# Performance work log

Hardware: AMD Instinct MI355X
Metric: run time of the kernel (lower is better)

## Reference

```python
import jax, jax.numpy as jnp
import numpy as np

WS = 32          # window_size -> N = WS*WS = 1024
DIM = 1024
HEADS = 16
BATCH = 16


def _local_mask():
    # token i maps to grid cell (i//WS, i%WS); attend iff within 3x3 neighborhood
    idx = jnp.arange(WS * WS)
    r, c = idx // WS, idx % WS
    return (jnp.abs(r[:, None] - r[None, :]) <= 1) & (jnp.abs(c[:, None] - c[None, :]) <= 1)


def setup_inputs() -> dict:
    key = jax.random.key(0)
    k1, k2, k3 = jax.random.split(key, 3)
    N = WS * WS
    x = jax.random.normal(k1, (BATCH, N, DIM), dtype=jnp.float32)
    w_qkv = jax.random.normal(k2, (3 * DIM, DIM), dtype=jnp.float32) * 0.02
    w_proj = jax.random.normal(k3, (DIM, DIM), dtype=jnp.float32) * 0.02
    b_proj = jnp.zeros((DIM,), dtype=jnp.float32)
    return {"x": x, "w_qkv": w_qkv, "w_proj": w_proj, "b_proj": b_proj}


def reference(x, w_qkv, w_proj, b_proj):
    B, N, C = x.shape
    H = HEADS
    D = C // H
    scale = D ** (-0.5)
    # qkv projection: torch Linear is x @ W^T
    qkv = (x @ w_qkv.T).reshape(B, N, 3, H, D).transpose(2, 0, 3, 1, 4)  # (3,B,H,N,D)
    q, k, v = qkv[0], qkv[1], qkv[2]
    attn = jnp.einsum('bhnd,bhmd->bhnm', q, k) * scale  # (B,H,N,N)
    mask = _local_mask()  # (N,N) bool
    attn = jnp.where(mask[None, None], attn, -jnp.inf)
    attn = jax.nn.softmax(attn, axis=-1)
    out = jnp.einsum('bhnm,bhmd->bhnd', attn, v)          # (B,H,N,D)
    out = out.transpose(0, 2, 1, 3).reshape(B, N, C)      # (B,N,C)
    return out @ w_proj.T + b_proj
```

## Files before the change

kernel.cpp:

```cpp
#include <hip/hip_runtime.h>
#include <hip/hip_bf16.h>
#include <stdint.h>


typedef __bf16 bf16;
typedef __bf16 bf16x4_t __attribute__((ext_vector_type(4)));
typedef __bf16 bf16x8_t __attribute__((ext_vector_type(8)));
typedef float f32x4_t __attribute__((ext_vector_type(4)));

static __device__ __forceinline__ void gload_lds16(const void* g, void* l) {
  __builtin_amdgcn_global_load_lds((__attribute__((address_space(1))) void*)g,
                                   (__attribute__((address_space(3))) void*)l,
                                   16, 0, 0);
}

static __device__ __forceinline__ void block_barrier() {
  asm volatile("" ::: "memory");
  __builtin_amdgcn_s_barrier();
  asm volatile("" ::: "memory");
}

__global__ void cvt_all(const float* __restrict__ x, const float* __restrict__ wq,
                        const float* __restrict__ wp, bf16* __restrict__ xb,
                        bf16* __restrict__ wqb, bf16* __restrict__ wpb) {
  constexpr int NX = 4194304, NWQ = 786432;
  int i = blockIdx.x * blockDim.x + threadIdx.x;
  const float* src; bf16* dst; int off;
  if (i < NX)            { src = x;  dst = xb;  off = i; }
  else if (i < NX + NWQ) { src = wq; dst = wqb; off = i - NX; }
  else                   { src = wp; dst = wpb; off = i - (NX + NWQ); }
  float4 v = reinterpret_cast<const float4*>(src)[off];
  bf16x4_t o;
  o[0] = (bf16)v.x; o[1] = (bf16)v.y; o[2] = (bf16)v.z; o[3] = (bf16)v.w;
  reinterpret_cast<bf16x4_t*>(dst)[off] = o;
}

template<int OUT_BF16>
__global__ __launch_bounds__(256, 2)
void gemm4w(const bf16* __restrict__ A, const bf16* __restrict__ Bm,
            void* __restrict__ Cout, const float* __restrict__ bias,
            int M, int N, int K) {
  constexpr int SLOT = 24576;
  extern __shared__ __align__(16) char lds[];

  const int tid = threadIdx.x;
  const int w = tid >> 6, lane = tid & 63;
  const int fr = lane & 15, g = lane >> 4;
  const int wr = w >> 1, wc = w & 1;

  const int nwg = gridDim.x * gridDim.y;
  int lid = blockIdx.y * gridDim.x + blockIdx.x;
  lid = (lid & 7) * (nwg >> 3) + (lid >> 3);
  const int bx = lid % gridDim.x, by = lid / gridDim.x;
  const int row0 = by * 256, col0 = bx * 128;

  const bf16* Ag = A + (size_t)row0 * K;
  const bf16* Bg = Bm + (size_t)col0 * K;
  const int srow = tid >> 2;
  const int scol = ((tid & 3) ^ ((tid >> 3) & 3)) * 8;
  const int nkt  = K >> 5;

  f32x4_t acc[8][4] = {};

  auto stage = [&](int kt, int slot) {
    const int kb = kt << 5;
    char* sb = lds + slot * SLOT;
#pragma unroll
    for (int n = 0; n < 4; ++n)
      gload_lds16(Ag + (size_t)(n * 64 + srow) * K + kb + scol,
                  sb + n * 4096 + tid * 16);
#pragma unroll
    for (int n = 0; n < 2; ++n)
      gload_lds16(Bg + (size_t)(n * 64 + srow) * K + kb + scol,
                  sb + 16384 + n * 4096 + tid * 16);
  };

  const int uxor = ((fr >> 1) & 3) << 4;

  stage(0, 0);
  stage(1, 1);
  asm volatile("s_waitcnt vmcnt(6)" ::: "memory");
  block_barrier();

  int sl = 0;
  for (int kt = 0; kt < nkt; ++kt) {
    const bool pf = (kt + 2 < nkt);
    int s2 = sl + 2; if (s2 >= 3) s2 -= 3;
    if (pf) stage(kt + 2, s2);
    const char* cA = lds + sl * SLOT;
    const char* cB = cA + 16384;

    bf16x8_t a0[4], a1[4], b0[2], b1[2];
    auto lda = [&](bf16x8_t (&dst)[4], int q) {
#pragma unroll
      for (int i = 0; i < 4; ++i) {
        const int row = wr * 128 + (q * 4 + i) * 16 + fr;
        dst[i] = *reinterpret_cast<const bf16x8_t*>(cA + (row << 6) + ((g << 4) ^ uxor));
      }
    };
    auto ldb = [&](bf16x8_t (&dst)[2], int q) {
#pragma unroll
      for (int j = 0; j < 2; ++j) {
        const int row = wc * 64 + (q * 2 + j) * 16 + fr;
        dst[j] = *reinterpret_cast<const bf16x8_t*>(cB + (row << 6) + ((g << 4) ^ uxor));
      }
    };

    lda(a0, 0);
    ldb(b0, 0);
#pragma unroll
    for (int i = 0; i < 4; ++i)
#pragma unroll
      for (int j = 0; j < 2; ++j)
        acc[i][j] = __builtin_amdgcn_mfma_f32_16x16x32_bf16(a0[i], b0[j], acc[i][j], 0, 0, 0);
    ldb(b1, 1);
#pragma unroll
    for (int i = 0; i < 4; ++i)
#pragma unroll
      for (int j = 0; j < 2; ++j)
        acc[i][2 + j] = __builtin_amdgcn_mfma_f32_16x16x32_bf16(a0[i], b1[j], acc[i][2 + j], 0, 0, 0);
    lda(a1, 1);
#pragma unroll
    for (int i = 0; i < 4; ++i)
#pragma unroll
      for (int j = 0; j < 2; ++j)
        acc[4 + i][2 + j] = __builtin_amdgcn_mfma_f32_16x16x32_bf16(
            a1[i], b1[j], acc[4 + i][2 + j], 0, 0, 0);
#pragma unroll
    for (int i = 0; i < 4; ++i)
#pragma unroll
      for (int j = 0; j < 2; ++j)
        acc[4 + i][j] = __builtin_amdgcn_mfma_f32_16x16x32_bf16(
            a1[i], b0[j], acc[4 + i][j], 0, 0, 0);

    if (pf) asm volatile("s_waitcnt vmcnt(6)" ::: "memory");
    else    asm volatile("s_waitcnt vmcnt(0)" ::: "memory");
    block_barrier();
    sl = (sl + 1 == 3) ? 0 : sl + 1;
  }

#pragma unroll
  for (int fm = 0; fm < 8; ++fm) {
    const int rbase = row0 + wr * 128 + fm * 16 + g * 4;
#pragma unroll
    for (int fn = 0; fn < 4; ++fn) {
      const int col = col0 + wc * 64 + fn * 16 + fr;
#pragma unroll
      for (int r = 0; r < 4; ++r) {
        const size_t idx = (size_t)(rbase + r) * N + col;
        if constexpr (OUT_BF16) {
          reinterpret_cast<bf16*>(Cout)[idx] = (bf16)acc[fm][fn][r];
        } else {
          reinterpret_cast<float*>(Cout)[idx] = acc[fm][fn][r] + bias[col];
        }
      }
    }
  }
}

__global__ __launch_bounds__(256)
void local_attn(const bf16* __restrict__ qkv, bf16* __restrict__ outp) {
  __shared__ __align__(16) char sK[12288];
  __shared__ __align__(16) char sV[12288];

  const int tid  = threadIdx.x;
  const int w = tid >> 6, lane = tid & 63;
  const int ch = lane & 7;
  const int bid = blockIdx.x;
  const int r = bid & 31, h = (bid >> 5) & 15, b = bid >> 9;

  const bf16* qkvb = qkv + (size_t)(b * 1024) * 3072 + h * 64;
  const int tokp = w * 8 + (lane >> 3);

#pragma unroll
  for (int u = 0; u < 3; ++u) {
    const int jrow = min(max(r - 1 + u, 0), 31);
    const size_t j = (size_t)(jrow * 32 + tokp);
    gload_lds16(qkvb + j * 3072 + 1024 + ch * 8, sK + u * 4096 + w * 1024 + (lane & 7) * 16 + (lane >> 3) * 128);
  }
#pragma unroll
  for (int u = 0; u < 3; ++u) {
    const int jrow = min(max(r - 1 + u, 0), 31);
    const size_t j = (size_t)(jrow * 32 + tokp);
    gload_lds16(qkvb + j * 3072 + 2048 + ch * 8, sV + u * 4096 + w * 1024 + (lane & 7) * 16 + (lane >> 3) * 128);
  }

  const int c = tokp, i = r * 32 + c;
  bf16x8_t qv = *reinterpret_cast<const bf16x8_t*>(qkvb + (size_t)i * 3072 + ch * 8);
  float qf[8];
#pragma unroll
  for (int e = 0; e < 8; ++e) qf[e] = (float)qv[e];

  __syncthreads();

  float s[9];
#pragma unroll
  for (int t = 0; t < 9; ++t) {
    const int dr = t / 3 - 1, dc = t % 3 - 1;
    const int rr = r + dr, cc = c + dc;
    const int ccl = min(max(cc, 0), 31);
    const int wtok = (dr + 1) * 32 + ccl;
    const bf16x8_t kvv = *reinterpret_cast<const bf16x8_t*>(sK + wtok * 128 + ch * 16);
    float ps = 0.f;
#pragma unroll
    for (int e = 0; e < 8; ++e) ps += qf[e] * (float)kvv[e];
    ps += __shfl_xor(ps, 1);
    ps += __shfl_xor(ps, 2);
    ps += __shfl_xor(ps, 4);
    const bool valid = (rr >= 0 && rr < 32 && cc >= 0 && cc < 32);
    s[t] = ps * 0.125f + (valid ? 0.f : -1e30f);
  }

  float mx = s[0];
#pragma unroll
  for (int t = 1; t < 9; ++t) mx = fmaxf(mx, s[t]);

  float denom = 0.f, o[8] = {};
#pragma unroll
  for (int t = 0; t < 9; ++t) {
    const int dr = t / 3 - 1, dc = t % 3 - 1;
    const int ccl = min(max(c + dc, 0), 31);
    const int wtok = (dr + 1) * 32 + ccl;
    const float p = __expf(s[t] - mx);
    denom += p;
    const bf16x8_t vvv = *reinterpret_cast<const bf16x8_t*>(sV + wtok * 128 + ch * 16);
#pragma unroll
    for (int e = 0; e < 8; ++e) o[e] += p * (float)vvv[e];
  }

  const float inv = 1.f / denom;
  bf16x8_t ov;
#pragma unroll
  for (int e = 0; e < 8; ++e) ov[e] = (bf16)(o[e] * inv);
  *reinterpret_cast<bf16x8_t*>(outp + (size_t)(b * 1024 + i) * 1024 + h * 64 + ch * 8) = ov;
}

extern "C" void kernel_launch(void* const* d_in, const int* in_sizes, int n_in,
                              void* d_out, int out_size, void* d_ws, size_t ws_size,
                              hipStream_t stream) {
  const float* x      = (const float*)d_in[0];
  const float* w_qkv  = (const float*)d_in[1];
  const float* w_proj = (const float*)d_in[2];
  const float* b_proj = (const float*)d_in[3];
  float* out = (float*)d_out;

  const size_t nx   = (size_t)16384 * 1024;
  const size_t nwq  = (size_t)3072 * 1024;
  const size_t nwp  = (size_t)1024 * 1024;
  const size_t nqkv = (size_t)16384 * 3072;

  bf16* x_bf  = (bf16*)d_ws;
  bf16* wq_bf = x_bf + nx;
  bf16* wp_bf = wq_bf + nwq;
  bf16* qkv   = wp_bf + nwp;
  bf16* attn  = qkv + nqkv;

  (void)hipFuncSetAttribute((const void*)&gemm4w<1>,
                            hipFuncAttributeMaxDynamicSharedMemorySize, 73728);
  (void)hipFuncSetAttribute((const void*)&gemm4w<0>,
                            hipFuncAttributeMaxDynamicSharedMemorySize, 73728);

  cvt_all<<<20480, 256, 0, stream>>>(x, w_qkv, w_proj, x_bf, wq_bf, wp_bf);

  gemm4w<1><<<dim3(3072 / 128, 16384 / 256), 256, 73728, stream>>>(
      x_bf, wq_bf, qkv, nullptr, 16384, 3072, 1024);

  local_attn<<<8192, 256, 0, stream>>>(qkv, attn);

  gemm4w<0><<<dim3(1024 / 128, 16384 / 256), 256, 73728, stream>>>(
      attn, wp_bf, out, b_proj, 16384, 1024, 1024);
}
```

Baseline: 212.8 us.

## Widen GEMM tile to 256x256 with 8 waves and double-buffered LDS

```diff
diff --git a/kernel.cpp b/kernel.cpp
--- a/kernel.cpp
+++ b/kernel.cpp
@@ -18,6 +18,12 @@
   asm volatile("" ::: "memory");
   __builtin_amdgcn_s_barrier();
   asm volatile("" ::: "memory");
+}
+
+template<int CTRL>
+static __device__ __forceinline__ float dpp_xor_add(float v) {
+  int x = __builtin_amdgcn_update_dpp(0, __float_as_int(v), CTRL, 0xF, 0xF, true);
+  return v + __int_as_float(x);
 }
 
 __global__ void cvt_all(const float* __restrict__ x, const float* __restrict__ wq,
@@ -36,23 +42,23 @@
 }
 
 template<int OUT_BF16>
-__global__ __launch_bounds__(256, 2)
-void gemm4w(const bf16* __restrict__ A, const bf16* __restrict__ Bm,
-            void* __restrict__ Cout, const float* __restrict__ bias,
-            int M, int N, int K) {
-  constexpr int SLOT = 24576;
+__global__ __launch_bounds__(512, 2)
+void gemm_bk32(const bf16* __restrict__ A, const bf16* __restrict__ Bm,
+               void* __restrict__ Cout, const float* __restrict__ bias,
+               int M, int N, int K) {
+  constexpr int SLOT = 32768;
   extern __shared__ __align__(16) char lds[];
 
   const int tid = threadIdx.x;
   const int w = tid >> 6, lane = tid & 63;
   const int fr = lane & 15, g = lane >> 4;
-  const int wr = w >> 1, wc = w & 1;
+  const int wr = w >> 2, wc = w & 3;
 
   const int nwg = gridDim.x * gridDim.y;
   int lid = blockIdx.y * gridDim.x + blockIdx.x;
   lid = (lid & 7) * (nwg >> 3) + (lid >> 3);
   const int bx = lid % gridDim.x, by = lid / gridDim.x;
-  const int row0 = by * 256, col0 = bx * 128;
+  const int row0 = by * 256, col0 = bx * 256;
 
   const bf16* Ag = A + (size_t)row0 * K;
   const bf16* Bg = Bm + (size_t)col0 * K;
@@ -65,30 +71,23 @@
   auto stage = [&](int kt, int slot) {
     const int kb = kt << 5;
     char* sb = lds + slot * SLOT;
-#pragma unroll
-    for (int n = 0; n < 4; ++n)
-      gload_lds16(Ag + (size_t)(n * 64 + srow) * K + kb + scol,
-                  sb + n * 4096 + tid * 16);
-#pragma unroll
-    for (int n = 0; n < 2; ++n)
-      gload_lds16(Bg + (size_t)(n * 64 + srow) * K + kb + scol,
-                  sb + 16384 + n * 4096 + tid * 16);
+    gload_lds16(Ag + (size_t)(srow) * K + kb + scol,       sb + tid * 16);
+    gload_lds16(Ag + (size_t)(128 + srow) * K + kb + scol, sb + 8192 + tid * 16);
+    gload_lds16(Bg + (size_t)(srow) * K + kb + scol,       sb + 16384 + tid * 16);
+    gload_lds16(Bg + (size_t)(128 + srow) * K + kb + scol, sb + 24576 + tid * 16);
   };
 
   const int uxor = ((fr >> 1) & 3) << 4;
 
   stage(0, 0);
   stage(1, 1);
-  asm volatile("s_waitcnt vmcnt(6)" ::: "memory");
+  asm volatile("s_waitcnt vmcnt(4)" ::: "memory");
   block_barrier();
 
-  int sl = 0;
   for (int kt = 0; kt < nkt; ++kt) {
+    const char* cA = lds + (kt & 1) * SLOT;
+    const char* cB = cA + 16384;
     const bool pf = (kt + 2 < nkt);
-    int s2 = sl + 2; if (s2 >= 3) s2 -= 3;
-    if (pf) stage(kt + 2, s2);
-    const char* cA = lds + sl * SLOT;
-    const char* cB = cA + 16384;
 
     bf16x8_t a0[4], a1[4], b0[2], b1[2];
     auto lda = [&](bf16x8_t (&dst)[4], int q) {
@@ -133,10 +132,11 @@
         acc[4 + i][j] = __builtin_amdgcn_mfma_f32_16x16x32_bf16(
             a1[i], b0[j], acc[4 + i][j], 0, 0, 0);
 
-    if (pf) asm volatile("s_waitcnt vmcnt(6)" ::: "memory");
-    else    asm volatile("s_waitcnt vmcnt(0)" ::: "memory");
     block_barrier();
-    sl = (sl + 1 == 3) ? 0 : sl + 1;
+    if (pf) stage(kt + 2, kt & 1);
+    if (kt < nkt - 2) asm volatile("s_waitcnt vmcnt(4)" ::: "memory");
+    else              asm volatile("s_waitcnt vmcnt(0)" ::: "memory");
+    block_barrier();
   }
 
 #pragma unroll
@@ -176,13 +176,15 @@
   for (int u = 0; u < 3; ++u) {
     const int jrow = min(max(r - 1 + u, 0), 31);
     const size_t j = (size_t)(jrow * 32 + tokp);
-    gload_lds16(qkvb + j * 3072 + 1024 + ch * 8, sK + u * 4096 + w * 1024 + (lane & 7) * 16 + (lane >> 3) * 128);
+    gload_lds16(qkvb + j * 3072 + 1024 + ch * 8,
+                sK + u * 4096 + w * 1024 + (lane & 7) * 16 + (lane >> 3) * 128);
   }
 #pragma unroll
   for (int u = 0; u < 3; ++u) {
     const int jrow = min(max(r - 1 + u, 0), 31);
     const size_t j = (size_t)(jrow * 32 + tokp);
-    gload_lds16(qkvb + j * 3072 + 2048 + ch * 8, sV + u * 4096 + w * 1024 + (lane & 7) * 16 + (lane >> 3) * 128);
+    gload_lds16(qkvb + j * 3072 + 2048 + ch * 8,
+                sV + u * 4096 + w * 1024 + (lane & 7) * 16 + (lane >> 3) * 128);
   }
 
   const int c = tokp, i = r * 32 + c;
@@ -204,8 +206,8 @@
     float ps = 0.f;
 #pragma unroll
     for (int e = 0; e < 8; ++e) ps += qf[e] * (float)kvv[e];
-    ps += __shfl_xor(ps, 1);
-    ps += __shfl_xor(ps, 2);
+    ps = dpp_xor_add<0xB1>(ps);
+    ps = dpp_xor_add<0x4E>(ps);
     ps += __shfl_xor(ps, 4);
     const bool valid = (rr >= 0 && rr < 32 && cc >= 0 && cc < 32);
     s[t] = ps * 0.125f + (valid ? 0.f : -1e30f);
@@ -255,18 +257,18 @@
   bf16* qkv   = wp_bf + nwp;
   bf16* attn  = qkv + nqkv;
 
-  (void)hipFuncSetAttribute((const void*)&gemm4w<1>,
-                            hipFuncAttributeMaxDynamicSharedMemorySize, 73728);
-  (void)hipFuncSetAttribute((const void*)&gemm4w<0>,
-                            hipFuncAttributeMaxDynamicSharedMemorySize, 73728);
+  (void)hipFuncSetAttribute((const void*)&gemm_bk32<1>,
+                            hipFuncAttributeMaxDynamicSharedMemorySize, 65536);
+  (void)hipFuncSetAttribute((const void*)&gemm_bk32<0>,
+                            hipFuncAttributeMaxDynamicSharedMemorySize, 65536);
 
   cvt_all<<<20480, 256, 0, stream>>>(x, w_qkv, w_proj, x_bf, wq_bf, wp_bf);
 
-  gemm4w<1><<<dim3(3072 / 128, 16384 / 256), 256, 73728, stream>>>(
+  gemm_bk32<1><<<dim3(3072 / 256, 16384 / 256), 512, 65536, stream>>>(
       x_bf, wq_bf, qkv, nullptr, 16384, 3072, 1024);
 
   local_attn<<<8192, 256, 0, stream>>>(qkv, attn);
 
-  gemm4w<0><<<dim3(1024 / 128, 16384 / 256), 256, 73728, stream>>>(
+  gemm_bk32<0><<<dim3(1024 / 256, 16384 / 256), 512, 65536, stream>>>(
       attn, wp_bf, out, b_proj, 16384, 1024, 1024);
 }
```

Result: no change. 209.0 us (-1.7%).
